# Kernel tuning notes

Measured on AMD Instinct MI355X. Metric: run time of the kernel, lower is better.

The kernel has to match this reference:

```python
import jax, jax.numpy as jnp
import numpy as np

N = 100000
E = 3200000
IN_C = 128
HID = 128


def setup_inputs() -> dict:
    key = jax.random.key(0)
    k1, k2, k3, k4, k5 = jax.random.split(key, 5)
    x = jax.random.normal(k1, (N, IN_C), dtype=jnp.float32)
    edge_index = jax.random.randint(k2, (2, E), 0, N, dtype=jnp.int64)
    edge_weight = jax.random.uniform(k3, (E,), dtype=jnp.float32)
    # GCNConv linear weight [out, in] (applied as x @ W.T), glorot-ish scale
    W = jax.random.normal(k4, (HID, IN_C), dtype=jnp.float32) / np.sqrt(IN_C)
    bias = jnp.zeros((HID,), dtype=jnp.float32)
    # PReLU per-channel alpha, torch default init 0.25
    alpha = jnp.full((HID,), 0.25, dtype=jnp.float32)
    return {"x": x, "edge_index": edge_index, "edge_weight": edge_weight,
            "W": W, "bias": bias, "alpha": alpha}


def reference(x, edge_index, edge_weight, W, bias, alpha):
    n = x.shape[0]
    # gcn_norm with self-loops (fill value 1.0)
    loop_idx = jnp.arange(n, dtype=edge_index.dtype)
    row = jnp.concatenate([edge_index[0], loop_idx])  # source
    col = jnp.concatenate([edge_index[1], loop_idx])  # target
    ew = jnp.concatenate([edge_weight, jnp.ones((n,), dtype=edge_weight.dtype)])
    deg = jax.ops.segment_sum(ew, col, num_segments=n)  # in-degree by weight
    dinv = jnp.where(deg > 0, jax.lax.rsqrt(deg), 0.0)
    norm = dinv[row] * ew * dinv[col]  # [E+N]
    # linear transform first (GCNConv order), then gather-scatter aggregation
    h = x @ W.T  # [N, HID]
    msgs = norm[:, None] * h[row]  # [E+N, HID]
    out = jax.ops.segment_sum(msgs, col, num_segments=n) + bias  # [N, HID]
    # PReLU with per-channel alpha
    return jnp.where(out > 0, out, alpha * out)
```

## Files before the change

kernel.cpp:

```cpp
#include <hip/hip_runtime.h>


#define NBLK    512
#define MAXBKT  2048
#define EPB     6250
#define P2T     512
#define QSCALE  32767.0f
#define Q9      511.0f
#define SBS     16

typedef float vfloat2 __attribute__((ext_vector_type(2)));

__device__ __forceinline__ unsigned bf16pack2(float a, float b) {
    unsigned ua = __float_as_uint(a);
    ua = (ua + 0x7fffu + ((ua >> 16) & 1u)) >> 16;
    unsigned ub = __float_as_uint(b);
    ub = (ub + 0x7fffu + ((ub >> 16) & 1u)) >> 16;
    return ua | (ub << 16);
}

__device__ __forceinline__ float2 bf16unpack2(unsigned u) {
    return make_float2(__uint_as_float(u << 16),
                       __uint_as_float(u & 0xffff0000u));
}

__device__ __forceinline__ int chunk_swz(int bid) {
    return (bid & 7) * (NBLK / 8) + (bid >> 3);
}

__global__ __launch_bounds__(256) void p1_hist(const int* __restrict__ col,
                                               unsigned* __restrict__ hist,
                                               int e, int nbkt, int epb) {
    __shared__ unsigned lh[MAXBKT];
    int c = chunk_swz(blockIdx.x);
    int t = threadIdx.x;
    for (int k = t; k < nbkt; k += 256) lh[k] = 0;
    __syncthreads();
    int s = c * epb, en = s + epb; if (en > e) en = e;
    for (int i = s + t; i < en; i += 256)
        atomicAdd(&lh[__builtin_nontemporal_load(&col[i]) >> 6], 1u);
    __syncthreads();
    for (int k = t; k < nbkt; k += 256)
        hist[(size_t)k * NBLK + c] = lh[k];
}

__global__ __launch_bounds__(1024) void scan_partial2(
    const unsigned* __restrict__ a, unsigned* __restrict__ part, int m) {
    __shared__ unsigned red[1024];
    int t = threadIdx.x, i = blockIdx.x * 1024 + t;
    red[t] = (i < m) ? a[i] : 0;
    __syncthreads();
    #pragma unroll
    for (int d = 512; d > 0; d >>= 1) {
        if (t < d) red[t] += red[t + d];
        __syncthreads();
    }
    if (t == 0) part[blockIdx.x] = red[0];
}

__global__ __launch_bounds__(1024) void scan_base2(
    unsigned* __restrict__ part, int nb, int* __restrict__ offs, int n, int e) {
    __shared__ unsigned s[1024];
    int t = threadIdx.x;
    unsigned v = (t < nb) ? part[t] : 0;
    s[t] = v;
    __syncthreads();
    for (int d = 1; d < 1024; d <<= 1) {
        unsigned add = (t >= d) ? s[t - d] : 0;
        __syncthreads();
        s[t] += add;
        __syncthreads();
    }
    if (t < nb) part[t] = s[t] - v;
    if (t == 0) offs[n] = e;
}

__global__ __launch_bounds__(1024) void scan_write2(
    unsigned* __restrict__ a, const unsigned* __restrict__ part, int m) {
    __shared__ unsigned s[1024];
    int t = threadIdx.x, i = blockIdx.x * 1024 + t;
    unsigned v = (i < m) ? a[i] : 0;
    s[t] = v;
    __syncthreads();
    for (int d = 1; d < 1024; d <<= 1) {
        unsigned add = (t >= d) ? s[t - d] : 0;
        __syncthreads();
        s[t] += add;
        __syncthreads();
    }
    if (i < m) a[i] = part[blockIdx.x] + s[t] - v;
}

__global__ __launch_bounds__(P2T) void p2_sort_scatter(
    const int* __restrict__ col, const int* __restrict__ row,
    const float* __restrict__ ew, const unsigned* __restrict__ base,
    unsigned* __restrict__ pay, int e, int nbkt, int epb, int m) {
    __shared__ unsigned lcnt[MAXBKT];
    __shared__ unsigned lcur[MAXBKT];
    __shared__ unsigned lbase[MAXBKT];
    __shared__ unsigned sums[P2T];
    __shared__ unsigned pay_l[EPB];
    __shared__ unsigned short bk_l[EPB];

    int c0 = chunk_swz(blockIdx.x);
    int t = threadIdx.x;
    for (int k = t; k < MAXBKT; k += P2T) { lcnt[k] = 0; lcur[k] = 0; }
    __syncthreads();
    for (int k = t; k < nbkt; k += P2T) {
        size_t f = (size_t)k * NBLK + c0;
        unsigned b  = base[f];
        unsigned nx = (f + 1 < (size_t)m) ? base[f + 1] : (unsigned)e;
        lbase[k] = b;
        lcnt[k]  = nx - b;
    }
    __syncthreads();

    int s0 = c0 * epb, en = s0 + epb; if (en > e) en = e;
    int cnt_tot = en - s0;

    unsigned loc0, loc1, loc2, loc3, ls;
    {
        int b0 = t * 4;
        loc0 = lcnt[b0]; loc1 = lcnt[b0 + 1];
        loc2 = lcnt[b0 + 2]; loc3 = lcnt[b0 + 3];
        ls = loc0 + loc1 + loc2 + loc3;
        sums[t] = ls;
    }
    __syncthreads();
    for (int d = 1; d < P2T; d <<= 1) {
        unsigned add = (t >= d) ? sums[t - d] : 0;
        __syncthreads();
        sums[t] += add;
        __syncthreads();
    }
    {
        unsigned run = sums[t] - ls;
        int b0 = t * 4;
        lcnt[b0] = run;           run += loc0;
        lcnt[b0 + 1] = run;       run += loc1;
        lcnt[b0 + 2] = run;       run += loc2;
        lcnt[b0 + 3] = run;
    }
    __syncthreads();

    for (int i = s0 + t; i < en; i += P2T) {
        int c = __builtin_nontemporal_load(&col[i]);
        int r = __builtin_nontemporal_load(&row[i]);
        float w = __builtin_nontemporal_load(&ew[i]);
        int bk = c >> 6;
        unsigned q = (unsigned)(w * Q9 + 0.5f);
        unsigned rk = atomicAdd(&lcur[bk], 1u);
        unsigned sl = lcnt[bk] + rk;
        pay_l[sl] = ((unsigned)(c & 63) << 26) | ((unsigned)r << 9) | q;
        bk_l[sl] = (unsigned short)bk;
    }
    __syncthreads();

    for (int sl = t; sl < cnt_tot; sl += P2T) {
        int bk = (int)bk_l[sl];
        unsigned g = lbase[bk] + (sl - lcnt[bk]);
        pay[g] = pay_l[sl];
    }
}

__global__ __launch_bounds__(256) void p3_build(
    const unsigned* __restrict__ pay,
    const unsigned* __restrict__ histBase,
    unsigned* __restrict__ csr, int* __restrict__ offs,
    float* __restrict__ dinv, int n, int nbkt, int e) {
    __shared__ unsigned cnt[64][SBS], lofs[64][SBS], cur[64][SBS];
    __shared__ unsigned wsum[64], tbase[64], ttot[64];
    int bk = blockIdx.x;
    int zs = (int)histBase[(size_t)bk * NBLK];
    int ze = (bk + 1 < nbkt) ? (int)histBase[(size_t)(bk + 1) * NBLK] : e;
    int t = threadIdx.x;
    for (int k = t; k < 64 * SBS; k += 256) {
        (&cnt[0][0])[k] = 0;
        (&cur[0][0])[k] = 0;
    }
    if (t < 64) wsum[t] = 0;
    __syncthreads();
    for (int p = zs + t; p < ze; p += 256) {
        unsigned v = pay[p];
        int l = (int)(v >> 26);
        int sb = (int)(((v >> 9) & 0x1ffffu) >> 13);
        atomicAdd(&cnt[l][sb], 1u);
        atomicAdd(&wsum[l], v & 0x1ffu);
    }
    __syncthreads();
    if (t < 64) {
        unsigned s = 0;
        #pragma unroll
        for (int j = 0; j < SBS; ++j) s += cnt[t][j];
        ttot[t] = s;
    }
    __syncthreads();
    if (t == 0) {
        unsigned run = 0;
        for (int l = 0; l < 64; ++l) { tbase[l] = run; run += ttot[l]; }
    }
    __syncthreads();
    if (t < 64) {
        unsigned run = tbase[t];
        #pragma unroll
        for (int j = 0; j < SBS; ++j) { lofs[t][j] = run; run += cnt[t][j]; }
    }
    __syncthreads();
    for (int p = zs + t; p < ze; p += 256) {
        unsigned v = pay[p];
        int l = (int)(v >> 26);
        unsigned lo = v & 0x03ffffffu;
        int sb = (int)((lo >> 9) >> 13);
        unsigned rk = atomicAdd(&cur[l][sb], 1u);
        csr[zs + lofs[l][sb] + rk] = lo;
    }
    if (t < 64) {
        int node = bk * 64 + t;
        if (node < n) {
            offs[node] = zs + (int)tbase[t];
            float dg = 1.0f + (float)wsum[t] * (1.0f / Q9);
            dinv[node] = rsqrtf(dg);
        }
    }
}

__global__ __launch_bounds__(256) void csr2_fill(const unsigned* __restrict__ csr,
                                                 const float* __restrict__ dinv,
                                                 unsigned* __restrict__ csr2, int e) {
    int i = blockIdx.x * 256 + threadIdx.x;
    if (i < e) {
        unsigned v = __builtin_nontemporal_load(&csr[i]);
        unsigned src = v >> 9;
        float a = dinv[src] * ((float)(v & 0x1ffu) * (1.0f / Q9));
        csr2[i] = (src << 15) | (unsigned)(a * QSCALE + 0.5f);
    }
}

__global__ __launch_bounds__(512) void gemm_kernel(const float* __restrict__ x,
                                                   const float* __restrict__ W,
                                                   unsigned* __restrict__ h, int n) {
    __shared__ float Wt[128][128];
    int t = threadIdx.x;
    const float4* W4 = (const float4*)W;
    #pragma unroll
    for (int it = 0; it < 8; ++it) {
        int i = t + it * 512;
        float4 v = W4[i];
        int o  = i >> 5;
        int kb = (i & 31) << 2;
        Wt[kb + 0][o ^ (((kb + 0) & 7) << 2)] = v.x;
        Wt[kb + 1][o ^ (((kb + 1) & 7) << 2)] = v.y;
        Wt[kb + 2][o ^ (((kb + 2) & 7) << 2)] = v.z;
        Wt[kb + 3][o ^ (((kb + 3) & 7) << 2)] = v.w;
    }
    __syncthreads();

    int tc = t & 31;
    int rs = t >> 5;
    int r0 = blockIdx.x * 128 + rs * 8;
    if (r0 >= n) return;
    const float4* x4 = (const float4*)x;

    float acc[8][4];
    #pragma unroll
    for (int ri = 0; ri < 8; ++ri)
        #pragma unroll
        for (int j = 0; j < 4; ++j) acc[ri][j] = 0.0f;

    int rcnt = n - r0; if (rcnt > 8) rcnt = 8;

    if (rcnt == 8) {
        for (int kq = 0; kq < 32; ++kq) {
            int kb = kq << 2;
            float4 wv0 = *(const float4*)&Wt[kb + 0][(4 * tc) ^ (((kb + 0) & 7) << 2)];
            float4 wv1 = *(const float4*)&Wt[kb + 1][(4 * tc) ^ (((kb + 1) & 7) << 2)];
            float4 wv2 = *(const float4*)&Wt[kb + 2][(4 * tc) ^ (((kb + 2) & 7) << 2)];
            float4 wv3 = *(const float4*)&Wt[kb + 3][(4 * tc) ^ (((kb + 3) & 7) << 2)];
            #pragma unroll
            for (int ri = 0; ri < 8; ++ri) {
                float4 xv = x4[(size_t)(r0 + ri) * 32 + kq];
                acc[ri][0] += xv.x * wv0.x + xv.y * wv1.x + xv.z * wv2.x + xv.w * wv3.x;
                acc[ri][1] += xv.x * wv0.y + xv.y * wv1.y + xv.z * wv2.y + xv.w * wv3.y;
                acc[ri][2] += xv.x * wv0.z + xv.y * wv1.z + xv.z * wv2.z + xv.w * wv3.z;
                acc[ri][3] += xv.x * wv0.w + xv.y * wv1.w + xv.z * wv2.w + xv.w * wv3.w;
            }
        }
        uint2* h2 = (uint2*)h;
        #pragma unroll
        for (int ri = 0; ri < 8; ++ri)
            h2[(size_t)(r0 + ri) * 32 + tc] =
                make_uint2(bf16pack2(acc[ri][0], acc[ri][1]),
                           bf16pack2(acc[ri][2], acc[ri][3]));
    } else {
        for (int kq = 0; kq < 32; ++kq) {
            int kb = kq << 2;
            float4 wv0 = *(const float4*)&Wt[kb + 0][(4 * tc) ^ (((kb + 0) & 7) << 2)];
            float4 wv1 = *(const float4*)&Wt[kb + 1][(4 * tc) ^ (((kb + 1) & 7) << 2)];
            float4 wv2 = *(const float4*)&Wt[kb + 2][(4 * tc) ^ (((kb + 2) & 7) << 2)];
            float4 wv3 = *(const float4*)&Wt[kb + 3][(4 * tc) ^ (((kb + 3) & 7) << 2)];
            for (int ri = 0; ri < rcnt; ++ri) {
                float4 xv = x4[(size_t)(r0 + ri) * 32 + kq];
                acc[ri][0] += xv.x * wv0.x + xv.y * wv1.x + xv.z * wv2.x + xv.w * wv3.x;
                acc[ri][1] += xv.x * wv0.y + xv.y * wv1.y + xv.z * wv2.y + xv.w * wv3.y;
                acc[ri][2] += xv.x * wv0.z + xv.y * wv1.z + xv.z * wv2.z + xv.w * wv3.z;
                acc[ri][3] += xv.x * wv0.w + xv.y * wv1.w + xv.z * wv2.w + xv.w * wv3.w;
            }
        }
        uint2* h2 = (uint2*)h;
        for (int ri = 0; ri < rcnt; ++ri)
            h2[(size_t)(r0 + ri) * 32 + tc] =
                make_uint2(bf16pack2(acc[ri][0], acc[ri][1]),
                           bf16pack2(acc[ri][2], acc[ri][3]));
    }
}

__global__ __launch_bounds__(256) void aggregate_kernel(
    const unsigned* __restrict__ h, const unsigned* __restrict__ csr2,
    const int* __restrict__ offs, const float* __restrict__ dinv,
    const float* __restrict__ bias, const float* __restrict__ alpha,
    float* __restrict__ out, int n, int swzq) {
    int bid = blockIdx.x;
    int sb  = swzq ? ((bid & 7) * swzq + (bid >> 3)) : bid;
    int w = sb * 4 + (threadIdx.x >> 6);
    if (w >= n) return;
    int lane = threadIdx.x & 63;

    int beg = __builtin_amdgcn_readfirstlane(offs[w]);
    int end = __builtin_amdgcn_readfirstlane(offs[w + 1]);
    float ax = 0.0f, ay = 0.0f;

    int i = beg;
    int end4 = beg + ((end - beg) & ~3);
    for (; i < end4; i += 4) {
        unsigned v0 = csr2[i];
        unsigned v1 = csr2[i + 1];
        unsigned v2 = csr2[i + 2];
        unsigned v3 = csr2[i + 3];
        unsigned u0 = h[(size_t)(v0 >> 15) * 64 + lane];
        unsigned u1 = h[(size_t)(v1 >> 15) * 64 + lane];
        unsigned u2 = h[(size_t)(v2 >> 15) * 64 + lane];
        unsigned u3 = h[(size_t)(v3 >> 15) * 64 + lane];
        float a0 = (float)(v0 & 0x7fffu) * (1.0f / QSCALE);
        float a1 = (float)(v1 & 0x7fffu) * (1.0f / QSCALE);
        float a2 = (float)(v2 & 0x7fffu) * (1.0f / QSCALE);
        float a3 = (float)(v3 & 0x7fffu) * (1.0f / QSCALE);
        float2 h0 = bf16unpack2(u0), h1 = bf16unpack2(u1);
        float2 h2 = bf16unpack2(u2), h3 = bf16unpack2(u3);
        ax += a0 * h0.x; ay += a0 * h0.y;
        ax += a1 * h1.x; ay += a1 * h1.y;
        ax += a2 * h2.x; ay += a2 * h2.y;
        ax += a3 * h3.x; ay += a3 * h3.y;
    }
    for (; i < end; ++i) {
        unsigned v = csr2[i];
        unsigned u = h[(size_t)(v >> 15) * 64 + lane];
        float a = (float)(v & 0x7fffu) * (1.0f / QSCALE);
        float2 hv = bf16unpack2(u);
        ax += a * hv.x; ay += a * hv.y;
    }

    float dc = dinv[w];
    float2 hc = bf16unpack2(h[(size_t)w * 64 + lane]);
    ax += dc * hc.x; ay += dc * hc.y;

    float2 bv = ((const float2*)bias)[lane];
    float2 av = ((const float2*)alpha)[lane];
    float ox = ax * dc + bv.x;
    float oy = ay * dc + bv.y;
    ox = ox > 0.0f ? ox : av.x * ox;
    oy = oy > 0.0f ? oy : av.y * oy;
    vfloat2 ov; ov.x = ox; ov.y = oy;
    __builtin_nontemporal_store(ov,
        (vfloat2*)&((float2*)out)[(size_t)w * 64 + lane]);
}

extern "C" void kernel_launch(void* const* d_in, const int* in_sizes, int n_in,
                              void* d_out, int out_size, void* d_ws, size_t ws_size,
                              hipStream_t stream) {
    const float* x     = (const float*)d_in[0];
    const int*   ei    = (const int*)d_in[1];
    const float* ew    = (const float*)d_in[2];
    const float* W     = (const float*)d_in[3];
    const float* bias  = (const float*)d_in[4];
    const float* alpha = (const float*)d_in[5];
    float* out = (float*)d_out;

    const int n = in_sizes[0] / 128;
    const int e = in_sizes[1] / 2;
    const int* row = ei;
    const int* col = ei + e;

    const int nbkt = (n + 63) >> 6;
    const int m    = nbkt * NBLK;
    const int epb  = (e + NBLK - 1) / NBLK;
    const int nb2  = (m + 1023) / 1024;

    char* ws = (char*)d_ws;
    size_t off = 0;
    auto alloc = [&](size_t bytes) -> char* {
        char* p = ws + off;
        off = (off + bytes + 255) & ~(size_t)255;
        return p;
    };
    unsigned* hist = (unsigned*)alloc((size_t)m * 4);
    unsigned* part = (unsigned*)alloc((size_t)1024 * 4);
    int*      offs = (int*)     alloc((size_t)(n + 1) * 4);
    float*    dinv = (float*)   alloc((size_t)n * 4);
    unsigned* pay  = (unsigned*)alloc((size_t)e * 4);
    unsigned* csr  = (unsigned*)alloc((size_t)e * 4);
    unsigned* csr2 = (unsigned*)alloc((size_t)e * 4);
    unsigned* h    = (unsigned*)alloc((size_t)n * 128 * 2);
    (void)ws_size; (void)n_in; (void)out_size;

    p1_hist<<<NBLK, 256, 0, stream>>>(col, hist, e, nbkt, epb);
    scan_partial2<<<nb2, 1024, 0, stream>>>(hist, part, m);
    scan_base2<<<1, 1024, 0, stream>>>(part, nb2, offs, n, e);
    scan_write2<<<nb2, 1024, 0, stream>>>(hist, part, m);
    p2_sort_scatter<<<NBLK, P2T, 0, stream>>>(col, row, ew, hist, pay,
                                              e, nbkt, epb, m);
    p3_build<<<nbkt, 256, 0, stream>>>(pay, hist, csr, offs, dinv, n, nbkt, e);
    csr2_fill<<<(e + 255) / 256, 256, 0, stream>>>(csr, dinv, csr2, e);

    int gg = (n + 127) / 128;
    gemm_kernel<<<gg, 512, 0, stream>>>(x, W, h, n);

    int ga = (n + 3) / 4;
    int swzq = (ga % 8 == 0) ? ga / 8 : 0;
    aggregate_kernel<<<ga, 256, 0, stream>>>(h, csr2, offs, dinv,
                                             bias, alpha, out, n, swzq);
}
```

Baseline: 268.5 us.

## Co-schedule sort scatter with GEMM and fold csr2 fill into split CSR build

Merges the p2 sort-scatter and the GEMM into one launch. Blocks are interleaved so that the sort blocks and the GEMM blocks share the GPU concurrently, with a unioned shared-memory buffer. The CSR build is split into a stats kernel that writes per-bucket offsets to global memory and a scatter kernel that writes the final quantized csr2 entries directly. This removes the intermediate csr array and the separate csr2_fill pass. The cost is an extra pass over pay, and the larger shared footprint of the fused kernel may limit occupancy for the GEMM blocks.

```diff
diff --git a/kernel.cpp b/kernel.cpp
--- a/kernel.cpp
+++ b/kernel.cpp
@@ -4,7 +4,6 @@
 #define NBLK    512
 #define MAXBKT  2048
 #define EPB     6250
-#define P2T     512
 #define QSCALE  32767.0f
 #define Q9      511.0f
 #define SBS     16
@@ -91,156 +90,89 @@
     if (i < m) a[i] = part[blockIdx.x] + s[t] - v;
 }
 
-__global__ __launch_bounds__(P2T) void p2_sort_scatter(
+__global__ __launch_bounds__(512) void fused_p2_gemm(
     const int* __restrict__ col, const int* __restrict__ row,
     const float* __restrict__ ew, const unsigned* __restrict__ base,
-    unsigned* __restrict__ pay, int e, int nbkt, int epb, int m) {
-    __shared__ unsigned lcnt[MAXBKT];
-    __shared__ unsigned lcur[MAXBKT];
-    __shared__ unsigned lbase[MAXBKT];
-    __shared__ unsigned sums[P2T];
-    __shared__ unsigned pay_l[EPB];
-    __shared__ unsigned short bk_l[EPB];
-
-    int c0 = chunk_swz(blockIdx.x);
+    unsigned* __restrict__ pay, int e, int nbkt, int epb, int m,
+    const float* __restrict__ x, const float* __restrict__ W,
+    unsigned* __restrict__ h, int n, int nblocks) {
+    __shared__ unsigned smem[16384];
+    int bid = blockIdx.x;
     int t = threadIdx.x;
-    for (int k = t; k < MAXBKT; k += P2T) { lcnt[k] = 0; lcur[k] = 0; }
-    __syncthreads();
-    for (int k = t; k < nbkt; k += P2T) {
-        size_t f = (size_t)k * NBLK + c0;
-        unsigned b  = base[f];
-        unsigned nx = (f + 1 < (size_t)m) ? base[f + 1] : (unsigned)e;
-        lbase[k] = b;
-        lcnt[k]  = nx - b;
-    }
-    __syncthreads();
-
-    int s0 = c0 * epb, en = s0 + epb; if (en > e) en = e;
-    int cnt_tot = en - s0;
-
-    unsigned loc0, loc1, loc2, loc3, ls;
-    {
-        int b0 = t * 4;
-        loc0 = lcnt[b0]; loc1 = lcnt[b0 + 1];
-        loc2 = lcnt[b0 + 2]; loc3 = lcnt[b0 + 3];
-        ls = loc0 + loc1 + loc2 + loc3;
-        sums[t] = ls;
-    }
-    __syncthreads();
-    for (int d = 1; d < P2T; d <<= 1) {
-        unsigned add = (t >= d) ? sums[t - d] : 0;
-        __syncthreads();
-        sums[t] += add;
-        __syncthreads();
-    }
-    {
-        unsigned run = sums[t] - ls;
-        int b0 = t * 4;
-        lcnt[b0] = run;           run += loc0;
-        lcnt[b0 + 1] = run;       run += loc1;
-        lcnt[b0 + 2] = run;       run += loc2;
-        lcnt[b0 + 3] = run;
-    }
-    __syncthreads();
-
-    for (int i = s0 + t; i < en; i += P2T) {
-        int c = __builtin_nontemporal_load(&col[i]);
-        int r = __builtin_nontemporal_load(&row[i]);
-        float w = __builtin_nontemporal_load(&ew[i]);
-        int bk = c >> 6;
-        unsigned q = (unsigned)(w * Q9 + 0.5f);
-        unsigned rk = atomicAdd(&lcur[bk], 1u);
-        unsigned sl = lcnt[bk] + rk;
-        pay_l[sl] = ((unsigned)(c & 63) << 26) | ((unsigned)r << 9) | q;
-        bk_l[sl] = (unsigned short)bk;
-    }
-    __syncthreads();
-
-    for (int sl = t; sl < cnt_tot; sl += P2T) {
-        int bk = (int)bk_l[sl];
-        unsigned g = lbase[bk] + (sl - lcnt[bk]);
-        pay[g] = pay_l[sl];
-    }
-}
-
-__global__ __launch_bounds__(256) void p3_build(
-    const unsigned* __restrict__ pay,
-    const unsigned* __restrict__ histBase,
-    unsigned* __restrict__ csr, int* __restrict__ offs,
-    float* __restrict__ dinv, int n, int nbkt, int e) {
-    __shared__ unsigned cnt[64][SBS], lofs[64][SBS], cur[64][SBS];
-    __shared__ unsigned wsum[64], tbase[64], ttot[64];
-    int bk = blockIdx.x;
-    int zs = (int)histBase[(size_t)bk * NBLK];
-    int ze = (bk + 1 < nbkt) ? (int)histBase[(size_t)(bk + 1) * NBLK] : e;
-    int t = threadIdx.x;
-    for (int k = t; k < 64 * SBS; k += 256) {
-        (&cnt[0][0])[k] = 0;
-        (&cur[0][0])[k] = 0;
-    }
-    if (t < 64) wsum[t] = 0;
-    __syncthreads();
-    for (int p = zs + t; p < ze; p += 256) {
-        unsigned v = pay[p];
-        int l = (int)(v >> 26);
-        int sb = (int)(((v >> 9) & 0x1ffffu) >> 13);
-        atomicAdd(&cnt[l][sb], 1u);
-        atomicAdd(&wsum[l], v & 0x1ffu);
-    }
-    __syncthreads();
-    if (t < 64) {
-        unsigned s = 0;
-        #pragma unroll
-        for (int j = 0; j < SBS; ++j) s += cnt[t][j];
-        ttot[t] = s;
-    }
-    __syncthreads();
-    if (t == 0) {
-        unsigned run = 0;
-        for (int l = 0; l < 64; ++l) { tbase[l] = run; run += ttot[l]; }
-    }
-    __syncthreads();
-    if (t < 64) {
-        unsigned run = tbase[t];
-        #pragma unroll
-        for (int j = 0; j < SBS; ++j) { lofs[t][j] = run; run += cnt[t][j]; }
-    }
-    __syncthreads();
-    for (int p = zs + t; p < ze; p += 256) {
-        unsigned v = pay[p];
-        int l = (int)(v >> 26);
-        unsigned lo = v & 0x03ffffffu;
-        int sb = (int)((lo >> 9) >> 13);
-        unsigned rk = atomicAdd(&cur[l][sb], 1u);
-        csr[zs + lofs[l][sb] + rk] = lo;
-    }
-    if (t < 64) {
-        int node = bk * 64 + t;
-        if (node < n) {
-            offs[node] = zs + (int)tbase[t];
-            float dg = 1.0f + (float)wsum[t] * (1.0f / Q9);
-            dinv[node] = rsqrtf(dg);
-        }
-    }
-}
-
-__global__ __launch_bounds__(256) void csr2_fill(const unsigned* __restrict__ csr,
-                                                 const float* __restrict__ dinv,
-                                                 unsigned* __restrict__ csr2, int e) {
-    int i = blockIdx.x * 256 + threadIdx.x;
-    if (i < e) {
-        unsigned v = __builtin_nontemporal_load(&csr[i]);
-        unsigned src = v >> 9;
-        float a = dinv[src] * ((float)(v & 0x1ffu) * (1.0f / Q9));
-        csr2[i] = (src << 15) | (unsigned)(a * QSCALE + 0.5f);
-    }
-}
-
-__global__ __launch_bounds__(512) void gemm_kernel(const float* __restrict__ x,
-                                                   const float* __restrict__ W,
-                                                   unsigned* __restrict__ h, int n) {
-    __shared__ float Wt[128][128];
-    int t = threadIdx.x;
+    unsigned p2b = (unsigned)(((unsigned long long)bid * NBLK) / nblocks);
+    bool isP2 = ((((unsigned long long)(bid + 1) * NBLK) / nblocks) > p2b);
+
+    if (isP2) {
+        unsigned* lcnt  = smem;
+        unsigned* lcur  = smem + 2048;
+        unsigned* lbase = smem + 4096;
+        unsigned* sums  = smem + 6144;
+        unsigned* pay_l = smem + 6656;
+        unsigned short* bk_l = (unsigned short*)(smem + 12906);
+
+        int c0 = (int)p2b;
+        for (int k = t; k < MAXBKT; k += 512) { lcnt[k] = 0; lcur[k] = 0; }
+        __syncthreads();
+        for (int k = t; k < nbkt; k += 512) {
+            size_t f = (size_t)k * NBLK + c0;
+            unsigned b  = base[f];
+            unsigned nx = (f + 1 < (size_t)m) ? base[f + 1] : (unsigned)e;
+            lbase[k] = b;
+            lcnt[k]  = nx - b;
+        }
+        __syncthreads();
+
+        int s0 = c0 * epb, en = s0 + epb; if (en > e) en = e;
+        int cnt_tot = en - s0;
+
+        unsigned loc0, loc1, loc2, loc3, ls;
+        {
+            int b0 = t * 4;
+            loc0 = lcnt[b0]; loc1 = lcnt[b0 + 1];
+            loc2 = lcnt[b0 + 2]; loc3 = lcnt[b0 + 3];
+            ls = loc0 + loc1 + loc2 + loc3;
+            sums[t] = ls;
+        }
+        __syncthreads();
+        for (int d = 1; d < 512; d <<= 1) {
+            unsigned add = (t >= d) ? sums[t - d] : 0;
+            __syncthreads();
+            sums[t] += add;
+            __syncthreads();
+        }
+        {
+            unsigned run = sums[t] - ls;
+            int b0 = t * 4;
+            lcnt[b0] = run;           run += loc0;
+            lcnt[b0 + 1] = run;       run += loc1;
+            lcnt[b0 + 2] = run;       run += loc2;
+            lcnt[b0 + 3] = run;
+        }
+        __syncthreads();
+
+        for (int i = s0 + t; i < en; i += 512) {
+            int c = __builtin_nontemporal_load(&col[i]);
+            int r = __builtin_nontemporal_load(&row[i]);
+            float w = __builtin_nontemporal_load(&ew[i]);
+            int bk = c >> 6;
+            unsigned q = (unsigned)(w * Q9 + 0.5f);
+            unsigned rk = atomicAdd(&lcur[bk], 1u);
+            unsigned sl = lcnt[bk] + rk;
+            pay_l[sl] = ((unsigned)(c & 63) << 26) | ((unsigned)r << 9) | q;
+            bk_l[sl] = (unsigned short)bk;
+        }
+        __syncthreads();
+
+        for (int sl = t; sl < cnt_tot; sl += 512) {
+            int bk = (int)bk_l[sl];
+            unsigned g = lbase[bk] + (sl - lcnt[bk]);
+            pay[g] = pay_l[sl];
+        }
+        return;
+    }
+
+    int gidx = bid - (int)p2b;
+    float (*Wt)[128] = (float (*)[128])smem;
     const float4* W4 = (const float4*)W;
     #pragma unroll
     for (int it = 0; it < 8; ++it) {
@@ -257,7 +189,7 @@
 
     int tc = t & 31;
     int rs = t >> 5;
-    int r0 = blockIdx.x * 128 + rs * 8;
+    int r0 = gidx * 128 + rs * 8;
     if (r0 >= n) return;
     const float4* x4 = (const float4*)x;
 
@@ -311,6 +243,80 @@
             h2[(size_t)(r0 + ri) * 32 + tc] =
                 make_uint2(bf16pack2(acc[ri][0], acc[ri][1]),
                            bf16pack2(acc[ri][2], acc[ri][3]));
+    }
+}
+
+__global__ __launch_bounds__(256) void p3a_stats(
+    const unsigned* __restrict__ pay, const unsigned* __restrict__ histBase,
+    unsigned short* __restrict__ lofsT, int* __restrict__ offs,
+    float* __restrict__ dinv, int n, int nbkt, int e) {
+    __shared__ unsigned cnt[64][SBS];
+    __shared__ unsigned wsum[64], tbase[64], ttot[64];
+    int bk = blockIdx.x;
+    int zs = (int)histBase[(size_t)bk * NBLK];
+    int ze = (bk + 1 < nbkt) ? (int)histBase[(size_t)(bk + 1) * NBLK] : e;
+    int t = threadIdx.x;
+    for (int k = t; k < 64 * SBS; k += 256) (&cnt[0][0])[k] = 0;
+    if (t < 64) wsum[t] = 0;
+    __syncthreads();
+    for (int p = zs + t; p < ze; p += 256) {
+        unsigned v = pay[p];
+        int l = (int)(v >> 26);
+        int sb = (int)(((v >> 9) & 0x1ffffu) >> 13);
+        atomicAdd(&cnt[l][sb], 1u);
+        atomicAdd(&wsum[l], v & 0x1ffu);
+    }
+    __syncthreads();
+    if (t < 64) {
+        unsigned s = 0;
+        #pragma unroll
+        for (int j = 0; j < SBS; ++j) s += cnt[t][j];
+        ttot[t] = s;
+    }
+    __syncthreads();
+    if (t == 0) {
+        unsigned run = 0;
+        for (int l = 0; l < 64; ++l) { tbase[l] = run; run += ttot[l]; }
+    }
+    __syncthreads();
+    if (t < 64) {
+        unsigned run = tbase[t];
+        unsigned short* dst = lofsT + ((size_t)bk * 64 + t) * SBS;
+        #pragma unroll
+        for (int j = 0; j < SBS; ++j) { dst[j] = (unsigned short)run; run += cnt[t][j]; }
+        int node = bk * 64 + t;
+        if (node < n) {
+            offs[node] = zs + (int)tbase[t];
+            float dg = 1.0f + (float)wsum[t] * (1.0f / Q9);
+            dinv[node] = rsqrtf(dg);
+        }
+    }
+}
+
+__global__ __launch_bounds__(256) void p3b_scatter(
+    const unsigned* __restrict__ pay, const unsigned* __restrict__ histBase,
+    const unsigned short* __restrict__ lofsT, const float* __restrict__ dinv,
+    unsigned* __restrict__ csr2, int nbkt, int e) {
+    __shared__ unsigned lofs[64][SBS];
+    __shared__ unsigned cur[64][SBS];
+    int bk = blockIdx.x;
+    int zs = (int)histBase[(size_t)bk * NBLK];
+    int ze = (bk + 1 < nbkt) ? (int)histBase[(size_t)(bk + 1) * NBLK] : e;
+    int t = threadIdx.x;
+    for (int k = t; k < 64 * SBS; k += 256) {
+        (&lofs[0][0])[k] = lofsT[(size_t)bk * 64 * SBS + k];
+        (&cur[0][0])[k] = 0;
+    }
+    __syncthreads();
+    for (int p = zs + t; p < ze; p += 256) {
+        unsigned v = pay[p];
+        int l = (int)(v >> 26);
+        unsigned src = (v >> 9) & 0x1ffffu;
+        int sb = (int)(src >> 13);
+        unsigned rk = atomicAdd(&cur[l][sb], 1u);
+        float a = dinv[src] * ((float)(v & 0x1ffu) * (1.0f / Q9));
+        csr2[zs + lofs[l][sb] + rk] =
+            (src << 15) | (unsigned)(a * QSCALE + 0.5f);
     }
 }
 
@@ -402,27 +408,30 @@
         off = (off + bytes + 255) & ~(size_t)255;
         return p;
     };
-    unsigned* hist = (unsigned*)alloc((size_t)m * 4);
-    unsigned* part = (unsigned*)alloc((size_t)1024 * 4);
-    int*      offs = (int*)     alloc((size_t)(n + 1) * 4);
-    float*    dinv = (float*)   alloc((size_t)n * 4);
-    unsigned* pay  = (unsigned*)alloc((size_t)e * 4);
-    unsigned* csr  = (unsigned*)alloc((size_t)e * 4);
-    unsigned* csr2 = (unsigned*)alloc((size_t)e * 4);
-    unsigned* h    = (unsigned*)alloc((size_t)n * 128 * 2);
+    unsigned*       hist  = (unsigned*)      alloc((size_t)m * 4);
+    unsigned*       part  = (unsigned*)      alloc((size_t)1024 * 4);
+    int*            offs  = (int*)           alloc((size_t)(n + 1) * 4);
+    float*          dinv  = (float*)         alloc((size_t)n * 4);
+    unsigned*       pay   = (unsigned*)      alloc((size_t)e * 4);
+    unsigned short* lofsT = (unsigned short*)alloc((size_t)nbkt * 64 * SBS * 2);
+    unsigned*       csr2  = (unsigned*)      alloc((size_t)e * 4);
+    unsigned*       h     = (unsigned*)      alloc((size_t)n * 128 * 2);
     (void)ws_size; (void)n_in; (void)out_size;
+
+    int gg = (n + 127) / 128;
+    int nblocks = NBLK + gg;
 
     p1_hist<<<NBLK, 256, 0, stream>>>(col, hist, e, nbkt, epb);
     scan_partial2<<<nb2, 1024, 0, stream>>>(hist, part, m);
     scan_base2<<<1, 1024, 0, stream>>>(part, nb2, offs, n, e);
     scan_write2<<<nb2, 1024, 0, stream>>>(hist, part, m);
-    p2_sort_scatter<<<NBLK, P2T, 0, stream>>>(col, row, ew, hist, pay,
-                                              e, nbkt, epb, m);
-    p3_build<<<nbkt, 256, 0, stream>>>(pay, hist, csr, offs, dinv, n, nbkt, e);
-    csr2_fill<<<(e + 255) / 256, 256, 0, stream>>>(csr, dinv, csr2, e);
-
-    int gg = (n + 127) / 128;
-    gemm_kernel<<<gg, 512, 0, stream>>>(x, W, h, n);
+    fused_p2_gemm<<<nblocks, 512, 0, stream>>>(col, row, ew, hist, pay,
+                                               e, nbkt, epb, m, x, W, h, n,
+                                               nblocks);
+    p3a_stats<<<nbkt, 256, 0, stream>>>(pay, hist, lofsT, offs, dinv,
+                                        n, nbkt, e);
+    p3b_scatter<<<nbkt, 256, 0, stream>>>(pay, hist, lofsT, dinv, csr2,
+                                          nbkt, e);
 
     int ga = (n + 3) / 4;
     int swzq = (ga % 8 == 0) ? ga / 8 : 0;
```

Result: slower. 325.2 us (+21.1%).
